# Optimization experiments

Measured on AMD Instinct MI355X. Metric: run time of the kernel, lower is better.

## Reference

```python
import jax, jax.numpy as jnp
import numpy as np

N_NODES = 65536
N_EDGES = 1048576


def gcn_conv(x, W, b, src, dst, n_nodes):
    """PyG GCNConv (normalize=True, add_self_loops already applied in src/dst):
    out = D^{-1/2} (A+I) D^{-1/2} X W + b, aggregated at dst (target) nodes."""
    deg = jax.ops.segment_sum(jnp.ones_like(dst, dtype=x.dtype), dst, num_segments=n_nodes)
    dis = jax.lax.rsqrt(jnp.maximum(deg, 1.0))  # self loops guarantee deg >= 1
    norm = dis[src] * dis[dst]                  # [E]
    h = x @ W                                   # [N, out]
    agg = jax.ops.segment_sum(h[src] * norm[:, None], dst, num_segments=n_nodes)
    return agg + b


def setup_inputs() -> dict:
    key = jax.random.key(0)
    ks = jax.random.split(key, 8)
    x = jax.random.normal(ks[0], (N_NODES, 128), dtype=jnp.float32)
    edge_index = jax.random.randint(ks[1], (2, N_EDGES), 0, N_NODES, dtype=jnp.int64)
    dims = [(128, 256), (256, 128), (128, 64)]
    params = {}
    for i, (din, dout) in enumerate(dims):
        scale = 1.0 / np.sqrt(din)
        params[f"W{i+1}"] = jax.random.uniform(ks[2 + i], (din, dout), dtype=jnp.float32, minval=-scale, maxval=scale)
        params[f"b{i+1}"] = jnp.zeros((dout,), dtype=jnp.float32)
    return {"x": x, "edge_index": edge_index, **params}


def reference(x, edge_index, W1, b1, W2, b2, W3, b3):
    n = x.shape[0]
    loop = jnp.arange(n, dtype=edge_index.dtype)
    src = jnp.concatenate([edge_index[0], loop])  # add self loops
    dst = jnp.concatenate([edge_index[1], loop])
    for W, b in ((W1, b1), (W2, b2), (W3, b3)):
        x = gcn_conv(x, W, b, src, dst, n)
        x = jax.nn.softmax(jax.nn.relu(x), axis=1)  # ReLU then Softmax(dim=1) per layer
    return x
```

## Files before the change

### kernel.cpp

```cpp
#include <hip/hip_runtime.h>
#include <cstdint>
#include <cstddef>

#define N_NODES 65536
#define N_EDGES 1048576
#define E_TOT   (N_EDGES + N_NODES)
#define CAP     5120

using short8  = __attribute__((ext_vector_type(8))) short;
using floatx4 = __attribute__((ext_vector_type(4))) float;
using half8   = __attribute__((ext_vector_type(8))) _Float16;
using half4   = __attribute__((ext_vector_type(4))) _Float16;
typedef unsigned short ushort_t;

__device__ inline void split_bf16(float a, short& hi, short& lo) {
    unsigned u  = __float_as_uint(a);
    unsigned hr = (u + 0x7fffu + ((u >> 16) & 1u)) >> 16;
    float    hf = __uint_as_float(hr << 16);
    hi = (short)hr;
    float    lf = a - hf;
    lo = (short)(__float_as_uint(lf) >> 16);
}


__global__ __launch_bounds__(1024) void k_bucket(const int* __restrict__ src, const int* __restrict__ dst,
                                                 int* __restrict__ gcur, unsigned* __restrict__ pk) {
    __shared__ int cnt[256];
    __shared__ int cur[256];
    int tid = threadIdx.x;
    if (tid < 256) cnt[tid] = 0;
    __syncthreads();
    int base = blockIdx.x * 4096;
    #pragma unroll
    for (int j = 0; j < 4; ++j) {
        int d = __builtin_nontemporal_load(&dst[base + j * 1024 + tid]);
        atomicAdd(&cnt[d >> 8], 1);
    }
    __syncthreads();
    if (tid < 256) cur[tid] = CAP * tid + atomicAdd(&gcur[tid], cnt[tid]);
    __syncthreads();
    #pragma unroll
    for (int j = 0; j < 4; ++j) {
        int e = base + j * 1024 + tid;
        int d = __builtin_nontemporal_load(&dst[e]);
        int s = __builtin_nontemporal_load(&src[e]);
        int pos = atomicAdd(&cur[d >> 8], 1);
        pk[pos] = ((unsigned)s << 16) | (unsigned)d;
    }
}

__global__ __launch_bounds__(256) void k_boff(const int* __restrict__ gcur, int* __restrict__ boff,
                                              int* __restrict__ off) {
    __shared__ int sb[256];
    int tid = threadIdx.x;
    int v = gcur[tid] + 256;
    sb[tid] = v;
    __syncthreads();
    #pragma unroll
    for (int s = 1; s < 256; s <<= 1) {
        int t = (tid >= s) ? sb[tid - s] : 0;
        __syncthreads();
        sb[tid] += t;
        __syncthreads();
    }
    boff[tid] = sb[tid] - v;
    if (tid == 255) boff[256] = sb[255];
    if (tid == 0) off[N_NODES] = E_TOT;
}

__global__ __launch_bounds__(1024) void k_sortb(const unsigned* __restrict__ pk, const int* __restrict__ gcur,
                                                const int* __restrict__ boff, int* __restrict__ off,
                                                float* __restrict__ dis, ushort_t* __restrict__ ssort) {
    __shared__ int cnt[256];
    __shared__ int sb[256];
    __shared__ int cur[256];
    int b = blockIdx.x;
    int tid = threadIdx.x;
    int n = gcur[b];
    const unsigned* p = pk + (size_t)b * CAP;
    if (tid < 256) cnt[tid] = 0;
    __syncthreads();
    for (int i = tid; i < n; i += 1024) atomicAdd(&cnt[p[i] & 255u], 1);
    __syncthreads();
    if (tid < 256) sb[tid] = cnt[tid];
    __syncthreads();
    #pragma unroll
    for (int s = 1; s < 256; s <<= 1) {
        int t = (tid < 256 && tid >= s) ? sb[tid - s] : 0;
        __syncthreads();
        if (tid < 256) sb[tid] += t;
        __syncthreads();
    }
    if (tid < 256) {
        int deg = cnt[tid];
        int o = boff[b] + (sb[tid] - deg) + tid;
        int d = b * 256 + tid;
        off[d] = o;
        dis[d] = rsqrtf((float)(deg + 1));
        ssort[o + deg] = (ushort_t)d;
        cur[tid] = o;
    }
    __syncthreads();
    for (int i = tid; i < n; i += 1024) {
        unsigned v = p[i];
        int pos = atomicAdd(&cur[v & 255u], 1);
        ssort[pos] = (ushort_t)(v >> 16);
    }
}


#define G1 (16 * 4 * 64)
#define G2 (8 * 8 * 64)
#define G3 (4 * 4 * 64)
#define NBX 8192
#define NBW ((G1 + G2 + G3 + 255) / 256)

__device__ inline void convw_split(const float* W, int K, int N, short* Bh, short* Bl, int g) {
    int lane = g & 63;
    int kt = (g >> 6) % (K / 32);
    int nt = (g >> 6) / (K / 32);
    int n = nt * 16 + (lane & 15);
    int kbase = kt * 32 + (lane >> 4) * 8;
    #pragma unroll
    for (int j = 0; j < 8; ++j) {
        short h, l;
        split_bf16(W[(size_t)(kbase + j) * N + n], h, l);
        Bh[(size_t)g * 8 + j] = h;
        Bl[(size_t)g * 8 + j] = l;
    }
}

__device__ inline void convw_h(const float* W, int K, int N, _Float16* Bf, int g) {
    int lane = g & 63;
    int kt = (g >> 6) % (K / 32);
    int nt = (g >> 6) / (K / 32);
    int n = nt * 16 + (lane & 15);
    int kbase = kt * 32 + (lane >> 4) * 8;
    #pragma unroll
    for (int j = 0; j < 8; ++j)
        Bf[(size_t)g * 8 + j] = (_Float16)W[(size_t)(kbase + j) * N + n];
}

__global__ __launch_bounds__(256) void k_fused(
        const float* __restrict__ x, const float* __restrict__ dis, _Float16* __restrict__ xh,
        const float* __restrict__ W1, short* __restrict__ w1h, short* __restrict__ w1l,
        const float* __restrict__ W2, _Float16* __restrict__ w2f,
        const float* __restrict__ W3, _Float16* __restrict__ w3f) {
    int b = blockIdx.x;
    if (b < NBX) {
        int idx = (b * 256 + threadIdx.x) * 4;
        int row = idx >> 7;
        float d = dis[row];
        float4 v = *(const float4*)(x + idx);
        half4 o = {(_Float16)(d * v.x), (_Float16)(d * v.y), (_Float16)(d * v.z), (_Float16)(d * v.w)};
        *(half4*)(xh + idx) = o;
    } else {
        int g = (b - NBX) * 256 + threadIdx.x;
        if (g < G1)                 convw_split(W1, 128, 256, w1h, w1l, g);
        else if (g < G1 + G2)       convw_h(W2, 256, 128, w2f, g - G1);
        else if (g < G1 + G2 + G3)  convw_h(W3, 128, 64, w3f, g - G1 - G2);
    }
}


template <int K, int N>
__global__ __launch_bounds__(256) void k_mms(const _Float16* __restrict__ A,
                                             const short* __restrict__ Bh, const short* __restrict__ Bl,
                                             const float* __restrict__ bias, _Float16* __restrict__ Cout) {
    constexpr int NT = N / 16;
    constexpr int KT = K / 32;
    int tid = threadIdx.x;
    int wave = tid >> 6, lane = tid & 63;
    int quad = lane >> 4, col = lane & 15;
    size_t row0 = (size_t)blockIdx.x * 64;
    const _Float16* ap = A + (row0 + wave * 16 + col) * K + quad * 8;

    floatx4 acc[NT];
    #pragma unroll
    for (int t = 0; t < NT; ++t) acc[t] = (floatx4)0.0f;

    for (int kt = 0; kt < KT; ++kt) {
        half8 a8 = *(const half8*)(ap + kt * 32);
        short ah[8], al[8];
        #pragma unroll
        for (int j = 0; j < 8; ++j) split_bf16((float)a8[j], ah[j], al[j]);
        short8 afh = *(short8*)ah;
        short8 afl = *(short8*)al;
        #pragma unroll
        for (int nt = 0; nt < NT; ++nt) {
            size_t bi = ((size_t)(nt * KT + kt) * 64 + lane);
            short8 bfh = ((const short8*)Bh)[bi];
            short8 bfl = ((const short8*)Bl)[bi];
            acc[nt] = __builtin_amdgcn_mfma_f32_16x16x32_bf16(afh, bfh, acc[nt], 0, 0, 0);
            acc[nt] = __builtin_amdgcn_mfma_f32_16x16x32_bf16(afh, bfl, acc[nt], 0, 0, 0);
            acc[nt] = __builtin_amdgcn_mfma_f32_16x16x32_bf16(afl, bfh, acc[nt], 0, 0, 0);
        }
    }

    size_t rbase = row0 + wave * 16 + quad * 4;
    float bv[NT];
    #pragma unroll
    for (int nt = 0; nt < NT; ++nt) bv[nt] = bias[nt * 16 + col];
    float mr[4] = {0.f, 0.f, 0.f, 0.f};
    #pragma unroll
    for (int nt = 0; nt < NT; ++nt)
        #pragma unroll
        for (int r = 0; r < 4; ++r) {
            float v = fmaxf(acc[nt][r] + bv[nt], 0.0f);
            acc[nt][r] = v;
            mr[r] = fmaxf(mr[r], v);
        }
    #pragma unroll
    for (int mask = 1; mask < 16; mask <<= 1)
        #pragma unroll
        for (int r = 0; r < 4; ++r) mr[r] = fmaxf(mr[r], __shfl_xor(mr[r], mask, 64));
    float sr[4] = {0.f, 0.f, 0.f, 0.f};
    #pragma unroll
    for (int nt = 0; nt < NT; ++nt)
        #pragma unroll
        for (int r = 0; r < 4; ++r) {
            float t = __expf(acc[nt][r] - mr[r]);
            acc[nt][r] = t;
            sr[r] += t;
        }
    #pragma unroll
    for (int mask = 1; mask < 16; mask <<= 1)
        #pragma unroll
        for (int r = 0; r < 4; ++r) sr[r] += __shfl_xor(sr[r], mask, 64);
    float inv[4];
    #pragma unroll
    for (int r = 0; r < 4; ++r) inv[r] = 1.0f / sr[r];
    #pragma unroll
    for (int nt = 0; nt < NT; ++nt)
        #pragma unroll
        for (int r = 0; r < 4; ++r)
            Cout[(rbase + r) * N + nt * 16 + col] = (_Float16)(acc[nt][r] * inv[r]);
}


template <int K, int N>
__global__ __launch_bounds__(256) void k_mmh(const _Float16* __restrict__ A,
                                             const _Float16* __restrict__ Bf,
                                             const float* __restrict__ dis, _Float16* __restrict__ Cout) {
    constexpr int NT = N / 16;
    constexpr int KT = K / 32;
    int tid = threadIdx.x;
    int wave = tid >> 6, lane = tid & 63;
    int quad = lane >> 4, col = lane & 15;
    size_t row0 = (size_t)blockIdx.x * 64;
    const _Float16* ap = A + (row0 + wave * 16 + col) * K + quad * 8;

    floatx4 acc[NT];
    #pragma unroll
    for (int t = 0; t < NT; ++t) acc[t] = (floatx4)0.0f;

    for (int kt = 0; kt < KT; ++kt) {
        half8 a8 = *(const half8*)(ap + kt * 32);
        #pragma unroll
        for (int nt = 0; nt < NT; ++nt) {
            half8 bf = ((const half8*)Bf)[(size_t)(nt * KT + kt) * 64 + lane];
            acc[nt] = __builtin_amdgcn_mfma_f32_16x16x32_f16(a8, bf, acc[nt], 0, 0, 0);
        }
    }

    size_t rbase = row0 + wave * 16 + quad * 4;
    float4 d4 = *(const float4*)(dis + rbase);
    float dr[4] = {d4.x, d4.y, d4.z, d4.w};
    #pragma unroll
    for (int nt = 0; nt < NT; ++nt)
        #pragma unroll
        for (int r = 0; r < 4; ++r)
            Cout[(rbase + r) * N + nt * 16 + col] = (_Float16)(acc[nt][r] * dr[r]);
}


template <int LPN, bool ACT, typename OutT>
__global__ __launch_bounds__(256) void k_aggq(const _Float16* __restrict__ h, const int* __restrict__ off,
                                              const ushort_t* __restrict__ ss, const float* __restrict__ dis,
                                              const float* __restrict__ bias, OutT* __restrict__ out) {
    constexpr int D = LPN * 8;
    constexpr int NPW = 64 / LPN;
    int lane = threadIdx.x & 63;
    int grp  = lane / LPN;
    int li   = lane & (LPN - 1);
    int c0   = li * 8;
    int n = (blockIdx.x * 4 + (threadIdx.x >> 6)) * NPW + grp;
    int e0 = off[n], e1 = off[n + 1];

    const _Float16* hb = h + c0;

    half8 hacc = {0, 0, 0, 0, 0, 0, 0, 0};
    float facc[8];
    #pragma unroll
    for (int j = 0; j < 8; ++j) facc[j] = 0.0f;

    int e = e0;
    for (; e + 4 <= e1; e += 4) {
        int s0 = ss[e];
        int s1 = ss[e + 1];
        int s2 = ss[e + 2];
        int s3 = ss[e + 3];
        half8 v0 = *(const half8*)(hb + (size_t)s0 * D);
        half8 v1 = *(const half8*)(hb + (size_t)s1 * D);
        half8 v2 = *(const half8*)(hb + (size_t)s2 * D);
        half8 v3 = *(const half8*)(hb + (size_t)s3 * D);
        half8 p = (v0 + v1) + (v2 + v3);
        if constexpr (ACT) {
            hacc += p;
        } else {
            #pragma unroll
            for (int j = 0; j < 8; ++j) facc[j] += (float)p[j];
        }
    }
    int rem = e1 - e;
    if (rem > 0) {
        int s0 = ss[e];
        half8 p = *(const half8*)(hb + (size_t)s0 * D);
        if (rem > 1) {
            int s1 = ss[e + 1];
            p += *(const half8*)(hb + (size_t)s1 * D);
        }
        if (rem > 2) {
            int s2 = ss[e + 2];
            p += *(const half8*)(hb + (size_t)s2 * D);
        }
        if constexpr (ACT) {
            hacc += p;
        } else {
            #pragma unroll
            for (int j = 0; j < 8; ++j) facc[j] += (float)p[j];
        }
    }
    if constexpr (ACT) {
        #pragma unroll
        for (int j = 0; j < 8; ++j) facc[j] = (float)hacc[j];
    }

    float dn = dis[n];
    if constexpr (ACT) {
        float m = 0.0f;
        #pragma unroll
        for (int j = 0; j < 8; ++j) {
            float v = fmaxf(fmaf(facc[j], dn, bias[c0 + j]), 0.0f);
            facc[j] = v;
            m = fmaxf(m, v);
        }
        #pragma unroll
        for (int mask = LPN / 2; mask > 0; mask >>= 1) m = fmaxf(m, __shfl_xor(m, mask, 64));
        float sum = 0.0f;
        #pragma unroll
        for (int j = 0; j < 8; ++j) {
            float t = __expf(facc[j] - m);
            facc[j] = t;
            sum += t;
        }
        #pragma unroll
        for (int mask = LPN / 2; mask > 0; mask >>= 1) sum += __shfl_xor(sum, mask, 64);
        float inv = 1.0f / sum;
        #pragma unroll
        for (int j = 0; j < 8; ++j) facc[j] *= inv;
    } else {
        #pragma unroll
        for (int j = 0; j < 8; ++j) facc[j] *= dn;
    }

    if constexpr (sizeof(OutT) == 2) {
        half8 o;
        #pragma unroll
        for (int j = 0; j < 8; ++j) o[j] = (_Float16)facc[j];
        *(half8*)((_Float16*)out + (size_t)n * D + c0) = o;
    } else {
        float* op = (float*)out + (size_t)n * D + c0;
        *(float4*)(op)     = make_float4(facc[0], facc[1], facc[2], facc[3]);
        *(float4*)(op + 4) = make_float4(facc[4], facc[5], facc[6], facc[7]);
    }
}


extern "C" void kernel_launch(void* const* d_in, const int* in_sizes, int n_in,
                              void* d_out, int out_size, void* d_ws, size_t ws_size,
                              hipStream_t stream) {
    const float* x  = (const float*)d_in[0];
    const int*   ei = (const int*)d_in[1];
    const float* W1 = (const float*)d_in[2];
    const float* b1 = (const float*)d_in[3];
    const float* W2 = (const float*)d_in[4];
    const float* b2 = (const float*)d_in[5];
    const float* W3 = (const float*)d_in[6];
    const float* b3 = (const float*)d_in[7];
    const int* srcE = ei;
    const int* dstE = ei + N_EDGES;

    char* p = (char*)d_ws;
    auto carve = [&](size_t bytes) {
        char* q = p;
        p += (bytes + 255) & ~(size_t)255;
        return q;
    };
    int*          gcur  = (int*)carve(sizeof(int) * 256);
    int*          boff  = (int*)carve(sizeof(int) * 257);
    int*          off   = (int*)carve(sizeof(int) * (N_NODES + 1));
    float*        dis   = (float*)carve(sizeof(float) * N_NODES);
    unsigned*     pk    = (unsigned*)carve(sizeof(unsigned) * 256 * CAP);
    ushort_t*     ssort = (ushort_t*)carve(sizeof(ushort_t) * E_TOT);
    short*        w1h   = (short*)carve(sizeof(short) * 128 * 256);
    short*        w1l   = (short*)carve(sizeof(short) * 128 * 256);
    _Float16*     w2f   = (_Float16*)carve(sizeof(_Float16) * 256 * 128);
    _Float16*     w3f   = (_Float16*)carve(sizeof(_Float16) * 128 * 64);
    _Float16*     xh    = (_Float16*)carve(sizeof(_Float16) * (size_t)N_NODES * 128);
    _Float16*     a0h   = (_Float16*)carve(sizeof(_Float16) * (size_t)N_NODES * 128);
    _Float16*     x1h   = (_Float16*)carve(sizeof(_Float16) * (size_t)N_NODES * 256);
    _Float16*     x2h   = (_Float16*)carve(sizeof(_Float16) * (size_t)N_NODES * 128);
    _Float16*     hh    = (_Float16*)carve(sizeof(_Float16) * (size_t)N_NODES * 128);

    (void)hipMemsetAsync(gcur, 0, sizeof(int) * 256, stream);
    k_bucket<<<256, 1024, 0, stream>>>(srcE, dstE, gcur, pk);
    k_boff<<<1, 256, 0, stream>>>(gcur, boff, off);
    k_sortb<<<256, 1024, 0, stream>>>(pk, gcur, boff, off, dis, ssort);
    k_fused<<<NBX + NBW, 256, 0, stream>>>(x, dis, xh, W1, w1h, w1l, W2, w2f, W3, w3f);

    k_aggq<16, false, _Float16><<<N_NODES / 16, 256, 0, stream>>>(xh, off, ssort, dis, nullptr, a0h);
    k_mms<128, 256><<<N_NODES / 64, 256, 0, stream>>>(a0h, w1h, w1l, b1, x1h);
    k_mmh<256, 128><<<N_NODES / 64, 256, 0, stream>>>(x1h, w2f, dis, hh);
    k_aggq<16, true, _Float16><<<N_NODES / 16, 256, 0, stream>>>(hh, off, ssort, dis, b2, x2h);
    k_mmh<128, 64><<<N_NODES / 64, 256, 0, stream>>>(x2h, w3f, dis, hh);
    k_aggq<8, true, float><<<N_NODES / 32, 256, 0, stream>>>(hh, off, ssort, dis, b3, (float*)d_out);
}
```

Baseline: 278.3 us.

## Fuse layer-1 GEMM+softmax with layer-2 GEMM through LDS; unroll aggregation by eight

After: 261.9 us. 1.06x faster.

```diff
diff --git a/kernel.cpp b/kernel.cpp
--- a/kernel.cpp
+++ b/kernel.cpp
@@ -163,23 +163,30 @@
 }
 
 
-template <int K, int N>
-__global__ __launch_bounds__(256) void k_mms(const _Float16* __restrict__ A,
-                                             const short* __restrict__ Bh, const short* __restrict__ Bl,
-                                             const float* __restrict__ bias, _Float16* __restrict__ Cout) {
-    constexpr int NT = N / 16;
-    constexpr int KT = K / 32;
+__global__ __launch_bounds__(256) void k_l12(const _Float16* __restrict__ A,
+        const short* __restrict__ Bh, const short* __restrict__ Bl,
+        const float* __restrict__ b1,
+        const _Float16* __restrict__ w2f,
+        const float* __restrict__ dis, _Float16* __restrict__ hh) {
+    constexpr int NT1 = 16;
+    constexpr int KT1 = 4;
+    constexpr int KT2 = 8;
+    constexpr int NT2 = 8;
+    constexpr int LSTR = 272;
+    __shared__ __align__(16) _Float16 xt[4][16][LSTR];
+
     int tid = threadIdx.x;
     int wave = tid >> 6, lane = tid & 63;
-    int quad = lane >> 4, col = lane & 15;
+    int quad = lane >> 4, li = lane & 15;
     size_t row0 = (size_t)blockIdx.x * 64;
-    const _Float16* ap = A + (row0 + wave * 16 + col) * K + quad * 8;
-
-    floatx4 acc[NT];
-    #pragma unroll
-    for (int t = 0; t < NT; ++t) acc[t] = (floatx4)0.0f;
-
-    for (int kt = 0; kt < KT; ++kt) {
+    const _Float16* ap = A + (row0 + wave * 16 + li) * 128 + quad * 8;
+
+    floatx4 acc[NT1];
+    #pragma unroll
+    for (int t = 0; t < NT1; ++t) acc[t] = (floatx4)0.0f;
+
+    #pragma unroll
+    for (int kt = 0; kt < KT1; ++kt) {
         half8 a8 = *(const half8*)(ap + kt * 32);
         short ah[8], al[8];
         #pragma unroll
@@ -187,54 +194,72 @@
         short8 afh = *(short8*)ah;
         short8 afl = *(short8*)al;
         #pragma unroll
-        for (int nt = 0; nt < NT; ++nt) {
-            size_t bi = ((size_t)(nt * KT + kt) * 64 + lane);
+        for (int nt = 0; nt < NT1; ++nt) {
+            size_t bi = ((size_t)(nt * KT1 + kt) * 64 + lane);
             short8 bfh = ((const short8*)Bh)[bi];
             short8 bfl = ((const short8*)Bl)[bi];
-            acc[nt] = __builtin_amdgcn_mfma_f32_16x16x32_bf16(afh, bfh, acc[nt], 0, 0, 0);
-            acc[nt] = __builtin_amdgcn_mfma_f32_16x16x32_bf16(afh, bfl, acc[nt], 0, 0, 0);
-            acc[nt] = __builtin_amdgcn_mfma_f32_16x16x32_bf16(afl, bfh, acc[nt], 0, 0, 0);
-        }
-    }
-
+            acc[nt] = __builtin_amdgcn_mfma_f32_16x16x32_bf16(bfh, afh, acc[nt], 0, 0, 0);
+            acc[nt] = __builtin_amdgcn_mfma_f32_16x16x32_bf16(bfl, afh, acc[nt], 0, 0, 0);
+            acc[nt] = __builtin_amdgcn_mfma_f32_16x16x32_bf16(bfh, afl, acc[nt], 0, 0, 0);
+        }
+    }
+
+    float mr = 0.0f;
+    #pragma unroll
+    for (int nt = 0; nt < NT1; ++nt) {
+        float4 bv = *(const float4*)(b1 + nt * 16 + quad * 4);
+        float bb[4] = {bv.x, bv.y, bv.z, bv.w};
+        #pragma unroll
+        for (int r = 0; r < 4; ++r) {
+            float v = fmaxf(acc[nt][r] + bb[r], 0.0f);
+            acc[nt][r] = v;
+            mr = fmaxf(mr, v);
+        }
+    }
+    mr = fmaxf(mr, __shfl_xor(mr, 16, 64));
+    mr = fmaxf(mr, __shfl_xor(mr, 32, 64));
+    float sum = 0.0f;
+    #pragma unroll
+    for (int nt = 0; nt < NT1; ++nt)
+        #pragma unroll
+        for (int r = 0; r < 4; ++r) {
+            float t = __expf(acc[nt][r] - mr);
+            acc[nt][r] = t;
+            sum += t;
+        }
+    sum += __shfl_xor(sum, 16, 64);
+    sum += __shfl_xor(sum, 32, 64);
+    float inv = 1.0f / sum;
+
+    _Float16* xrow = &xt[wave][li][0];
+    #pragma unroll
+    for (int nt = 0; nt < NT1; ++nt) {
+        half4 h4 = {(_Float16)(acc[nt][0] * inv), (_Float16)(acc[nt][1] * inv),
+                    (_Float16)(acc[nt][2] * inv), (_Float16)(acc[nt][3] * inv)};
+        *(half4*)(xrow + nt * 16 + quad * 4) = h4;
+    }
+    __syncthreads();
+
+    floatx4 acc2[NT2];
+    #pragma unroll
+    for (int t = 0; t < NT2; ++t) acc2[t] = (floatx4)0.0f;
+    #pragma unroll
+    for (int kt = 0; kt < KT2; ++kt) {
+        half8 a8 = *(const half8*)(xrow + kt * 32 + quad * 8);
+        #pragma unroll
+        for (int nt = 0; nt < NT2; ++nt) {
+            half8 bf = ((const half8*)w2f)[(size_t)(nt * KT2 + kt) * 64 + lane];
+            acc2[nt] = __builtin_amdgcn_mfma_f32_16x16x32_f16(a8, bf, acc2[nt], 0, 0, 0);
+        }
+    }
     size_t rbase = row0 + wave * 16 + quad * 4;
-    float bv[NT];
-    #pragma unroll
-    for (int nt = 0; nt < NT; ++nt) bv[nt] = bias[nt * 16 + col];
-    float mr[4] = {0.f, 0.f, 0.f, 0.f};
-    #pragma unroll
-    for (int nt = 0; nt < NT; ++nt)
-        #pragma unroll
-        for (int r = 0; r < 4; ++r) {
-            float v = fmaxf(acc[nt][r] + bv[nt], 0.0f);
-            acc[nt][r] = v;
-            mr[r] = fmaxf(mr[r], v);
-        }
-    #pragma unroll
-    for (int mask = 1; mask < 16; mask <<= 1)
-        #pragma unroll
-        for (int r = 0; r < 4; ++r) mr[r] = fmaxf(mr[r], __shfl_xor(mr[r], mask, 64));
-    float sr[4] = {0.f, 0.f, 0.f, 0.f};
-    #pragma unroll
-    for (int nt = 0; nt < NT; ++nt)
-        #pragma unroll
-        for (int r = 0; r < 4; ++r) {
-            float t = __expf(acc[nt][r] - mr[r]);
-            acc[nt][r] = t;
-            sr[r] += t;
-        }
-    #pragma unroll
-    for (int mask = 1; mask < 16; mask <<= 1)
-        #pragma unroll
-        for (int r = 0; r < 4; ++r) sr[r] += __shfl_xor(sr[r], mask, 64);
-    float inv[4];
-    #pragma unroll
-    for (int r = 0; r < 4; ++r) inv[r] = 1.0f / sr[r];
-    #pragma unroll
-    for (int nt = 0; nt < NT; ++nt)
+    float4 d4 = *(const float4*)(dis + rbase);
+    float dr[4] = {d4.x, d4.y, d4.z, d4.w};
+    #pragma unroll
+    for (int nt = 0; nt < NT2; ++nt)
         #pragma unroll
         for (int r = 0; r < 4; ++r)
-            Cout[(rbase + r) * N + nt * 16 + col] = (_Float16)(acc[nt][r] * inv[r]);
+            hh[(rbase + r) * 128 + nt * 16 + li] = (_Float16)(acc2[nt][r] * dr[r]);
 }
 
 
@@ -290,11 +315,41 @@
     const _Float16* hb = h + c0;
 
     half8 hacc = {0, 0, 0, 0, 0, 0, 0, 0};
+    half8 hacc2 = {0, 0, 0, 0, 0, 0, 0, 0};
     float facc[8];
     #pragma unroll
     for (int j = 0; j < 8; ++j) facc[j] = 0.0f;
 
     int e = e0;
+    for (; e + 8 <= e1; e += 8) {
+        int s0 = ss[e];
+        int s1 = ss[e + 1];
+        int s2 = ss[e + 2];
+        int s3 = ss[e + 3];
+        int s4 = ss[e + 4];
+        int s5 = ss[e + 5];
+        int s6 = ss[e + 6];
+        int s7 = ss[e + 7];
+        half8 v0 = *(const half8*)(hb + (size_t)s0 * D);
+        half8 v1 = *(const half8*)(hb + (size_t)s1 * D);
+        half8 v2 = *(const half8*)(hb + (size_t)s2 * D);
+        half8 v3 = *(const half8*)(hb + (size_t)s3 * D);
+        half8 v4 = *(const half8*)(hb + (size_t)s4 * D);
+        half8 v5 = *(const half8*)(hb + (size_t)s5 * D);
+        half8 v6 = *(const half8*)(hb + (size_t)s6 * D);
+        half8 v7 = *(const half8*)(hb + (size_t)s7 * D);
+        half8 p0 = (v0 + v1) + (v2 + v3);
+        half8 p1 = (v4 + v5) + (v6 + v7);
+        if constexpr (ACT) {
+            hacc  += p0;
+            hacc2 += p1;
+        } else {
+            #pragma unroll
+            for (int j = 0; j < 8; ++j) facc[j] += (float)p0[j];
+            #pragma unroll
+            for (int j = 0; j < 8; ++j) facc[j] += (float)p1[j];
+        }
+    }
     for (; e + 4 <= e1; e += 4) {
         int s0 = ss[e];
         int s1 = ss[e + 1];
@@ -332,6 +387,7 @@
         }
     }
     if constexpr (ACT) {
+        hacc += hacc2;
         #pragma unroll
         for (int j = 0; j < 8; ++j) facc[j] = (float)hacc[j];
     }
@@ -409,7 +465,6 @@
     _Float16*     w3f   = (_Float16*)carve(sizeof(_Float16) * 128 * 64);
     _Float16*     xh    = (_Float16*)carve(sizeof(_Float16) * (size_t)N_NODES * 128);
     _Float16*     a0h   = (_Float16*)carve(sizeof(_Float16) * (size_t)N_NODES * 128);
-    _Float16*     x1h   = (_Float16*)carve(sizeof(_Float16) * (size_t)N_NODES * 256);
     _Float16*     x2h   = (_Float16*)carve(sizeof(_Float16) * (size_t)N_NODES * 128);
     _Float16*     hh    = (_Float16*)carve(sizeof(_Float16) * (size_t)N_NODES * 128);
 
@@ -420,8 +475,7 @@
     k_fused<<<NBX + NBW, 256, 0, stream>>>(x, dis, xh, W1, w1h, w1l, W2, w2f, W3, w3f);
 
     k_aggq<16, false, _Float16><<<N_NODES / 16, 256, 0, stream>>>(xh, off, ssort, dis, nullptr, a0h);
-    k_mms<128, 256><<<N_NODES / 64, 256, 0, stream>>>(a0h, w1h, w1l, b1, x1h);
-    k_mmh<256, 128><<<N_NODES / 64, 256, 0, stream>>>(x1h, w2f, dis, hh);
+    k_l12<<<N_NODES / 64, 256, 0, stream>>>(a0h, w1h, w1l, b1, w2f, dis, hh);
     k_aggq<16, true, _Float16><<<N_NODES / 16, 256, 0, stream>>>(hh, off, ssort, dis, b2, x2h);
     k_mmh<128, 64><<<N_NODES / 64, 256, 0, stream>>>(x2h, w3f, dis, hh);
     k_aggq<8, true, float><<<N_NODES / 32, 256, 0, stream>>>(hh, off, ssort, dis, b3, (float*)d_out);
```
